# Kernel tuning notes

Measured on AMD Instinct MI355X. Metric: run time of the kernel, lower is better.

The kernel has to match this reference:

```python
import jax, jax.numpy as jnp
import numpy as np

N = 30000
E = 600000
IN = 64
HID = 128
EPS = 1e-5
HEADS_PER_LAYER = (4, 4, 1)


def _bn(x, g, b):
    # eval-mode BatchNorm: running_mean=0, running_var=1
    return x * (g / np.sqrt(1.0 + EPS)) + b


def _segment_softmax(e, dst, n):
    m = jax.ops.segment_max(e, dst, num_segments=n)
    ex = jnp.exp(e - m[dst])
    s = jax.ops.segment_sum(ex, dst, num_segments=n)
    return ex / (s[dst] + 1e-16)


def _gcn_conv(x, w, b, src, dst, norm, n):
    m = (x @ w)[src] * norm[:, None]            # [E+N, HID]
    return jax.ops.segment_sum(m, dst, num_segments=n) + b


def _gat_conv(x, w, a_src, a_dst, b, src, dst, n, heads):
    C = HID // heads
    xh = (x @ w).reshape(n, heads, C)
    asrc = (xh * a_src.reshape(heads, C)).sum(-1)   # [N, heads]
    adst = (xh * a_dst.reshape(heads, C)).sum(-1)
    e = jax.nn.leaky_relu(asrc[src] + adst[dst], 0.2)  # [E+N, heads]
    alpha = _segment_softmax(e, dst, n)
    out = jax.ops.segment_sum(xh[src] * alpha[:, :, None], dst, num_segments=n)
    return out.reshape(n, HID) + b


def _forward(x, gcn_in_w, gcn_in_b, gcn_res_w, gcn_res_b, gcn_w, gcn_b,
             gcn_bn_g, gcn_bn_b, gcn_c1w, gcn_c1b, gcn_c2w, gcn_c2b,
             gcn_c3w, gcn_c3b, gat_in_w, gat_in_b, gat_w, gat_asrc,
             gat_adst, gat_b, gat_bn_g, gat_bn_b, feat_imp, gat_c1w,
             gat_c1b, gat_cbn_g, gat_cbn_b, gat_c2w, gat_c2b, gat_c3w,
             gat_c3b, fin_w, fin_b, fin_bn_g, fin_bn_b, fin2_w, fin2_b,
             edge_index):
    n = x.shape[0]
    loop = jnp.arange(n, dtype=edge_index.dtype)
    src = jnp.concatenate([edge_index[0], loop])  # add self-loops
    dst = jnp.concatenate([edge_index[1], loop])
    # GCN symmetric normalization (with self-loops)
    deg = jax.ops.segment_sum(jnp.ones_like(dst, dtype=x.dtype), dst, num_segments=n)
    dis = jnp.where(deg > 0, jax.lax.rsqrt(jnp.maximum(deg, 1.0)), 0.0)
    norm = dis[src] * dis[dst]

    # ---- GCN branch (eval: dropout = identity, self-attn skipped since N>5000) ----
    xp = x @ gcn_in_w + gcn_in_b
    res = x @ gcn_res_w + gcn_res_b
    for i in range(3):
        xn = _gcn_conv(xp, gcn_w[i], gcn_b[i], src, dst, norm, n)
        xn = jax.nn.relu(_bn(xn, gcn_bn_g[i], gcn_bn_b[i]))
        if i % 2 == 1:
            xp = xn + res
            res = xp
        else:
            xp = xn
    h = jax.nn.relu(xp @ gcn_c1w + gcn_c1b)
    h = jax.nn.relu(h @ gcn_c2w + gcn_c2b)
    gcn_out = h @ gcn_c3w + gcn_c3b

    # ---- GAT branch ----
    xg = x @ gat_in_w + gat_in_b
    for i in range(3):
        xg = _gat_conv(xg, gat_w[i], gat_asrc[i], gat_adst[i], gat_b[i],
                       src, dst, n, HEADS_PER_LAYER[i])
        xg = jax.nn.elu(_bn(xg, gat_bn_g[i], gat_bn_b[i]))
    xg = xg * feat_imp
    h = jax.nn.relu(xg @ gat_c1w + gat_c1b)
    h = _bn(h, gat_cbn_g, gat_cbn_b)
    h = jax.nn.relu(h @ gat_c2w + gat_c2b)
    gat_out = h @ gat_c3w + gat_c3b

    # ---- fusion: N > 10000 -> weighted blend path ----
    fused = 0.6 * gcn_out + 0.4 * gat_out
    h = jax.nn.relu(fused @ fin_w + fin_b)
    h = _bn(h, fin_bn_g, fin_bn_b)
    return h @ fin2_w + fin2_b  # [N, 2]


def setup_inputs() -> dict:
    key = jax.random.key(0)
    ks = iter(jax.random.split(key, 64))

    def nrm(shape, scale=1.0):
        return jax.random.normal(next(ks), shape, dtype=jnp.float32) * scale

    s_in = 1.0 / np.sqrt(IN)
    s_h = 1.0 / np.sqrt(HID)
    inp = {}
    inp['x'] = nrm((N, IN))
    inp['edge_index'] = jax.random.randint(next(ks), (2, E), 0, N, dtype=jnp.int32)
    inp['gcn_in_w'] = nrm((IN, HID), s_in); inp['gcn_in_b'] = nrm((HID,), 0.01)
    inp['gcn_res_w'] = nrm((IN, HID), s_in); inp['gcn_res_b'] = nrm((HID,), 0.01)
    inp['gcn_w'] = nrm((3, HID, HID), s_h); inp['gcn_b'] = nrm((3, HID), 0.01)
    inp['gcn_bn_g'] = 1.0 + nrm((3, HID), 0.1); inp['gcn_bn_b'] = nrm((3, HID), 0.1)
    inp['gcn_c1w'] = nrm((HID, 64), s_h); inp['gcn_c1b'] = nrm((64,), 0.01)
    inp['gcn_c2w'] = nrm((64, 32), 0.125); inp['gcn_c2b'] = nrm((32,), 0.01)
    inp['gcn_c3w'] = nrm((32, HID), 0.18); inp['gcn_c3b'] = nrm((HID,), 0.01)
    inp['gat_in_w'] = nrm((IN, HID), s_in); inp['gat_in_b'] = nrm((HID,), 0.01)
    inp['gat_w'] = nrm((3, HID, HID), s_h)
    inp['gat_asrc'] = nrm((3, HID), s_h); inp['gat_adst'] = nrm((3, HID), s_h)
    inp['gat_b'] = nrm((3, HID), 0.01)
    inp['gat_bn_g'] = 1.0 + nrm((3, HID), 0.1); inp['gat_bn_b'] = nrm((3, HID), 0.1)
    inp['feat_imp'] = 1.0 + nrm((HID,), 0.1)
    inp['gat_c1w'] = nrm((HID, 64), s_h); inp['gat_c1b'] = nrm((64,), 0.01)
    inp['gat_cbn_g'] = 1.0 + nrm((64,), 0.1); inp['gat_cbn_b'] = nrm((64,), 0.1)
    inp['gat_c2w'] = nrm((64, 32), 0.125); inp['gat_c2b'] = nrm((32,), 0.01)
    inp['gat_c3w'] = nrm((32, HID), 0.18); inp['gat_c3b'] = nrm((HID,), 0.01)
    inp['fin_w'] = nrm((HID, 64), s_h); inp['fin_b'] = nrm((64,), 0.01)
    inp['fin_bn_g'] = 1.0 + nrm((64,), 0.1); inp['fin_bn_b'] = nrm((64,), 0.1)
    inp['fin2_w'] = nrm((64, 2), 0.125); inp['fin2_b'] = nrm((2,), 0.01)
    return inp


def reference(x, edge_index, gcn_in_w, gcn_in_b, gcn_res_w, gcn_res_b, gcn_w,
              gcn_b, gcn_bn_g, gcn_bn_b, gcn_c1w, gcn_c1b, gcn_c2w, gcn_c2b,
              gcn_c3w, gcn_c3b, gat_in_w, gat_in_b, gat_w, gat_asrc, gat_adst,
              gat_b, gat_bn_g, gat_bn_b, feat_imp, gat_c1w, gat_c1b, gat_cbn_g,
              gat_cbn_b, gat_c2w, gat_c2b, gat_c3w, gat_c3b, fin_w, fin_b,
              fin_bn_g, fin_bn_b, fin2_w, fin2_b):
    return _forward(x, gcn_in_w, gcn_in_b, gcn_res_w, gcn_res_b, gcn_w, gcn_b,
                    gcn_bn_g, gcn_bn_b, gcn_c1w, gcn_c1b, gcn_c2w, gcn_c2b,
                    gcn_c3w, gcn_c3b, gat_in_w, gat_in_b, gat_w, gat_asrc,
                    gat_adst, gat_b, gat_bn_g, gat_bn_b, feat_imp, gat_c1w,
                    gat_c1b, gat_cbn_g, gat_cbn_b, gat_c2w, gat_c2b, gat_c3w,
                    gat_c3b, fin_w, fin_b, fin_bn_g, fin_bn_b, fin2_w, fin2_b,
                    edge_index)
```

## Files before the change

### kernel.cpp

```cpp
#include <hip/hip_runtime.h>
#include <hip/hip_fp16.h>

#define RSQ_BN 0.9999950000374997f

typedef _Float16 f16x8 __attribute__((ext_vector_type(8)));
typedef float f32x4 __attribute__((ext_vector_type(4)));

union H8u { uint4 u4; __half h[8]; };
union H4u { uint2 u2; __half h[4]; };

__device__ __forceinline__ float leaky02(float x) { return x > 0.f ? x : 0.2f * x; }

__device__ __forceinline__ float4 ld4(const float* p) {
    return *reinterpret_cast<const float4*>(p);
}
__device__ __forceinline__ void ld8(float* d, const float* p) {
    float4 u = ld4(p), v = ld4(p + 4);
    d[0] = u.x; d[1] = u.y; d[2] = u.z; d[3] = u.w;
    d[4] = v.x; d[5] = v.y; d[6] = v.z; d[7] = v.w;
}


__global__ void hist_k(const int* __restrict__ edst, int* __restrict__ cnt, int E, int EN) {
    int i = blockIdx.x * 256 + threadIdx.x;
    if (i >= EN) return;
    int d = (i < E) ? edst[i] : (i - E);
    atomicAdd(&cnt[d], 1);
}

__global__ __launch_bounds__(256)
void scanA_k(const int* __restrict__ cnt, int* __restrict__ rowptr,
             int* __restrict__ bsum, int n) {
    __shared__ int sh[256];
    int t = threadIdx.x;
    int i = blockIdx.x * 256 + t;
    int v = (i < n) ? cnt[i] : 0;
    sh[t] = v;
    __syncthreads();
#pragma unroll
    for (int off = 1; off < 256; off <<= 1) {
        int u = 0;
        if (t >= off) u = sh[t - off];
        __syncthreads();
        sh[t] += u;
        __syncthreads();
    }
    if (i < n) rowptr[i] = sh[t] - v;
    if (t == 255) bsum[blockIdx.x] = sh[255];
}

__global__ __launch_bounds__(256)
void scanB_k(int* __restrict__ bsum, int nb) {
    __shared__ int sh[256];
    int t = threadIdx.x;
    int v = (t < nb) ? bsum[t] : 0;
    sh[t] = v;
    __syncthreads();
#pragma unroll
    for (int off = 1; off < 256; off <<= 1) {
        int u = 0;
        if (t >= off) u = sh[t - off];
        __syncthreads();
        sh[t] += u;
        __syncthreads();
    }
    if (t < nb) bsum[t] = sh[t] - v;
}

__global__ __launch_bounds__(256)
void scanC_k(const int* __restrict__ cnt, const int* __restrict__ bsum,
             int* __restrict__ rowptr, int* __restrict__ cursor,
             float* __restrict__ dis, int n, int EN) {
    int i = blockIdx.x * 256 + threadIdx.x;
    if (i < n) {
        int r = rowptr[i] + bsum[blockIdx.x];
        rowptr[i] = r;
        cursor[i] = r;
        dis[i] = rsqrtf((float)cnt[i]);
    }
    if (i == 0) rowptr[n] = EN;
}

__global__ void scatter_k(const int* __restrict__ esrc, const int* __restrict__ edst,
                          int* __restrict__ cursor, int* __restrict__ colidx, int E, int EN) {
    int i = blockIdx.x * 256 + threadIdx.x;
    if (i >= EN) return;
    int s, d;
    if (i < E) { s = esrc[i]; d = edst[i]; }
    else       { s = i - E; d = s; }
    int pos = atomicAdd(&cursor[d], 1);
    colidx[pos] = s;
}


__global__ void wtx_all_k(const float* __restrict__ gcn_in_w, const float* __restrict__ gcn_res_w,
                          const float* __restrict__ gat_in_w,
                          const float* __restrict__ gcn_w, const float* __restrict__ gat_w,
                          const float* __restrict__ gcn_c1w, const float* __restrict__ gat_c1w,
                          const float* __restrict__ gcn_c3w, const float* __restrict__ gat_c3w,
                          const float* __restrict__ fin_w,
                          const float* __restrict__ gcn_c2w, const float* __restrict__ gat_c2w,
                          const float* __restrict__ gat_asrc, const float* __restrict__ gat_adst,
                          __half* __restrict__ WTin, __half* __restrict__ WTg,
                          __half* __restrict__ WTa, __half* __restrict__ WTc1,
                          __half* __restrict__ WTc3, __half* __restrict__ WTfin,
                          __half* __restrict__ WTc2, __half* __restrict__ WTd) {
    int idx = blockIdx.x * 256 + threadIdx.x;
    const float* src;
    __half* dst;
    int K, M, o;
    if (idx < 24576) {
        int mi = idx >> 13; o = idx & 8191;
        src = mi == 0 ? gcn_in_w : (mi == 1 ? gcn_res_w : gat_in_w);
        dst = WTin + mi * 8192; K = 64; M = 128;
    } else if (idx < 73728) {
        int r = idx - 24576; int mi = r >> 14; o = r & 16383;
        src = gcn_w + mi * 16384; dst = WTg + mi * 16384; K = 128; M = 128;
    } else if (idx < 122880) {
        int r = idx - 73728; int mi = r >> 14; o = r & 16383;
        src = gat_w + mi * 16384; dst = WTa + mi * 16384; K = 128; M = 128;
    } else if (idx < 139264) {
        int r = idx - 122880; int mi = r >> 13; o = r & 8191;
        src = mi ? gat_c1w : gcn_c1w; dst = WTc1 + mi * 8192; K = 128; M = 64;
    } else if (idx < 147456) {
        int r = idx - 139264; int mi = r >> 12; o = r & 4095;
        src = mi ? gat_c3w : gcn_c3w; dst = WTc3 + mi * 4096; K = 32; M = 128;
    } else if (idx < 155648) {
        o = idx - 147456; src = fin_w; dst = WTfin; K = 128; M = 64;
    } else if (idx < 159744) {
        int r = idx - 155648; int mi = r >> 11; o = r & 2047;
        src = mi ? gat_c2w : gcn_c2w; dst = WTc2 + mi * 2048; K = 64; M = 32;
    } else if (idx < 165888) {
        int r = idx - 159744;
        int layer = r >> 11; o = r & 2047;
        int col = o >> 7, k = o & 127;
        int hh = (layer < 2) ? 4 : 1;
        int C = 128 / hh;
        float v = 0.f;
        if (col < hh) {
            const float* w = gat_w + (size_t)(layer * 128 + k) * 128 + col * C;
            const float* av = gat_asrc + layer * 128 + col * C;
            for (int c2 = 0; c2 < C; ++c2) v += w[c2] * av[c2];
        } else if (col >= 8 && col < 8 + hh) {
            int hthis = col - 8;
            const float* w = gat_w + (size_t)(layer * 128 + k) * 128 + hthis * C;
            const float* av = gat_adst + layer * 128 + hthis * C;
            for (int c2 = 0; c2 < C; ++c2) v += w[c2] * av[c2];
        }
        WTd[(size_t)layer * 2048 + o] = (__half)v;
        return;
    } else return;
    int mcol = o / K, k = o - mcol * K;
    dst[o] = (__half)src[k * M + mcol];
}


__device__ __forceinline__ f16x8 mk_af(const float* xr, int kb) {
    float4 v0 = ld4(xr + kb), v1 = ld4(xr + kb + 4);
    f16x8 af;
    af[0] = (_Float16)v0.x; af[1] = (_Float16)v0.y;
    af[2] = (_Float16)v0.z; af[3] = (_Float16)v0.w;
    af[4] = (_Float16)v1.x; af[5] = (_Float16)v1.y;
    af[6] = (_Float16)v1.z; af[7] = (_Float16)v1.w;
    return af;
}

__global__ __launch_bounds__(256)
void mfma_lin3_k(const float* __restrict__ X, const __half* __restrict__ WTin,
                 const float* __restrict__ b0, __half* __restrict__ Y0,
                 const float* __restrict__ b1, __half* __restrict__ Y1,
                 const float* __restrict__ b2, __half* __restrict__ Y2,
                 int n, int gper) {
    constexpr int K = 64, CT = 8;
    int set = blockIdx.x / gper, blk = blockIdx.x % gper;
    const __half* WT = WTin + (size_t)set * 8192;
    const float* bi = set == 0 ? b0 : (set == 1 ? b1 : b2);
    __half* Y = set == 0 ? Y0 : (set == 1 ? Y1 : Y2);
    int wave = threadIdx.x >> 6, lane = threadIdx.x & 63;
    int m = lane & 15, quad = lane >> 4;
    int row0 = blk * 64 + wave * 16;
    int arow = min(row0 + m, n - 1);
    const float* xr = X + (size_t)arow * K;
    f32x4 acc[CT];
#pragma unroll
    for (int ct = 0; ct < CT; ++ct) acc[ct] = (f32x4){0.f, 0.f, 0.f, 0.f};
#pragma unroll
    for (int k32 = 0; k32 < K / 32; ++k32) {
        int kb = k32 * 32 + quad * 8;
        f16x8 af = mk_af(xr, kb);
#pragma unroll
        for (int ct = 0; ct < CT; ++ct) {
            f16x8 bf = *reinterpret_cast<const f16x8*>(WT + (size_t)(ct * 16 + m) * K + kb);
            acc[ct] = __builtin_amdgcn_mfma_f32_16x16x32_f16(bf, af, acc[ct], 0, 0, 0);
        }
    }
    int row = row0 + m;
    if (row < n) {
#pragma unroll
        for (int ct = 0; ct < CT; ++ct) {
            int col = ct * 16 + quad * 4;
            float4 bv = ld4(bi + col);
            H4u w;
            w.h[0] = (__half)(acc[ct][0] + bv.x);
            w.h[1] = (__half)(acc[ct][1] + bv.y);
            w.h[2] = (__half)(acc[ct][2] + bv.z);
            w.h[3] = (__half)(acc[ct][3] + bv.w);
            *reinterpret_cast<uint2*>(Y + (size_t)row * 128 + col) = w.u2;
        }
    }
}


__global__ __launch_bounds__(256)
void dual128_mfma_k(const __half* __restrict__ Xg, const __half* __restrict__ WTg,
                    __half* __restrict__ Yg,
                    const __half* __restrict__ Xa, const __half* __restrict__ WTa,
                    __half* __restrict__ Ya,
                    const float* __restrict__ dis,
                    const __half* __restrict__ WTd,
                    float* __restrict__ avp, float* __restrict__ bvp,
                    int hh, int n, int gper) {
    bool gat = blockIdx.x >= gper;
    int blk = gat ? blockIdx.x - gper : blockIdx.x;
    const __half* X = gat ? Xa : Xg;
    const __half* WT = gat ? WTa : WTg;
    __half* Y = gat ? Ya : Yg;
    int wave = threadIdx.x >> 6;
    int lane = threadIdx.x & 63;
    int m = lane & 15, quad = lane >> 4;
    int row0 = blk * 64 + wave * 16;
    int arow = min(row0 + m, n - 1);
    const __half* xr = X + (size_t)arow * 128;
    f32x4 acc[8];
#pragma unroll
    for (int ct = 0; ct < 8; ++ct) acc[ct] = (f32x4){0.f, 0.f, 0.f, 0.f};
    int row = row0 + m;
    if (!gat) {
#pragma unroll
        for (int k32 = 0; k32 < 4; ++k32) {
            int kb = k32 * 32 + quad * 8;
            f16x8 af = *reinterpret_cast<const f16x8*>(xr + kb);
#pragma unroll
            for (int ct = 0; ct < 8; ++ct) {
                f16x8 bf = *reinterpret_cast<const f16x8*>(WT + (size_t)(ct * 16 + m) * 128 + kb);
                acc[ct] = __builtin_amdgcn_mfma_f32_16x16x32_f16(bf, af, acc[ct], 0, 0, 0);
            }
        }
        if (row < n) {
            float dv = dis[row];
#pragma unroll
            for (int ct = 0; ct < 8; ++ct) {
                int col = ct * 16 + quad * 4;
                H4u w;
                w.h[0] = (__half)(acc[ct][0] * dv);
                w.h[1] = (__half)(acc[ct][1] * dv);
                w.h[2] = (__half)(acc[ct][2] * dv);
                w.h[3] = (__half)(acc[ct][3] * dv);
                *reinterpret_cast<uint2*>(Y + (size_t)row * 128 + col) = w.u2;
            }
        }
    } else {
        f32x4 accd = (f32x4){0.f, 0.f, 0.f, 0.f};
#pragma unroll
        for (int k32 = 0; k32 < 4; ++k32) {
            int kb = k32 * 32 + quad * 8;
            f16x8 af = *reinterpret_cast<const f16x8*>(xr + kb);
#pragma unroll
            for (int ct = 0; ct < 8; ++ct) {
                f16x8 bf = *reinterpret_cast<const f16x8*>(WT + (size_t)(ct * 16 + m) * 128 + kb);
                acc[ct] = __builtin_amdgcn_mfma_f32_16x16x32_f16(bf, af, acc[ct], 0, 0, 0);
            }
            f16x8 bd = *reinterpret_cast<const f16x8*>(WTd + (size_t)m * 128 + kb);
            accd = __builtin_amdgcn_mfma_f32_16x16x32_f16(bd, af, accd, 0, 0, 0);
        }
        if (row < n) {
#pragma unroll
            for (int ct = 0; ct < 8; ++ct) {
                int col = ct * 16 + quad * 4;
                H4u w;
                w.h[0] = (__half)acc[ct][0];
                w.h[1] = (__half)acc[ct][1];
                w.h[2] = (__half)acc[ct][2];
                w.h[3] = (__half)acc[ct][3];
                *reinterpret_cast<uint2*>(Y + (size_t)row * 128 + col) = w.u2;
            }
            if (quad == 0) {
#pragma unroll
                for (int reg = 0; reg < 4; ++reg)
                    if (reg < hh) avp[row * hh + reg] = accd[reg];
            } else if (quad == 2) {
#pragma unroll
                for (int reg = 0; reg < 4; ++reg)
                    if (reg < hh) bvp[row * hh + reg] = accd[reg];
            }
        }
    }
}


__global__ __launch_bounds__(256)
void fused_gather_k(const int* __restrict__ rowptr, const int* __restrict__ colidx,
                    const float* __restrict__ dis,
                    const __half* __restrict__ Tg, const float* __restrict__ gbias,
                    const float* __restrict__ gbng, const float* __restrict__ gbnb,
                    const __half* __restrict__ res, __half* __restrict__ Yg,
                    const __half* __restrict__ Ta, const float* __restrict__ avp,
                    const float* __restrict__ bvp, const float* __restrict__ abias,
                    const float* __restrict__ abng, const float* __restrict__ abnb,
                    const float* __restrict__ fimp, __half* __restrict__ Ya,
                    int n, int hh, int log2C) {
    int idx = blockIdx.x * 256 + threadIdx.x;
    int i = idx >> 4;
    if (i >= n) return;
    int c = (idx & 15) * 8;
    int h = c >> log2C;
    float ad = bvp[i * hh + h];
    int p0 = rowptr[i], p1 = rowptr[i + 1];
    float g[8], a[8];
#pragma unroll
    for (int t = 0; t < 8; ++t) { g[t] = 0.f; a[t] = 0.f; }
    float m = -3.0e38f, s = 0.f;

    int ng = (p1 - p0 + 3) >> 2;
    int p = p0;
    int sx[4]; float av[4], vm[4];
#pragma unroll
    for (int j = 0; j < 4; ++j) {
        int q = p0 + j;
        vm[j] = (q < p1) ? 1.f : 0.f;
        sx[j] = colidx[min(q, p1 - 1)];
    }
#pragma unroll
    for (int j = 0; j < 4; ++j) av[j] = avp[sx[j] * hh + h];

    for (int gi = 0; gi < ng; ++gi) {
        uint4 qg[4], qa[4];
#pragma unroll
        for (int j = 0; j < 4; ++j)
            qg[j] = *reinterpret_cast<const uint4*>(Tg + (size_t)sx[j] * 128 + c);
#pragma unroll
        for (int j = 0; j < 4; ++j)
            qa[j] = *reinterpret_cast<const uint4*>(Ta + (size_t)sx[j] * 128 + c);
        int pn = p + 4;
        int sn[4]; float avn[4], vmn[4];
#pragma unroll
        for (int j = 0; j < 4; ++j) {
            int q = pn + j;
            vmn[j] = (q < p1) ? 1.f : 0.f;
            sn[j] = colidx[min(max(q, p0), p1 - 1)];
        }
#pragma unroll
        for (int j = 0; j < 4; ++j) avn[j] = avp[sn[j] * hh + h];
        float e0 = vm[0] > 0.f ? leaky02(av[0] + ad) : -3.0e38f;
        float e1 = vm[1] > 0.f ? leaky02(av[1] + ad) : -3.0e38f;
        float e2 = vm[2] > 0.f ? leaky02(av[2] + ad) : -3.0e38f;
        float e3 = vm[3] > 0.f ? leaky02(av[3] + ad) : -3.0e38f;
        float mc = fmaxf(fmaxf(e0, e1), fmaxf(e2, e3));
        float mn = fmaxf(m, mc);
        float scale = __expf(m - mn);
        float w0 = __expf(e0 - mn), w1 = __expf(e1 - mn);
        float w2 = __expf(e2 - mn), w3 = __expf(e3 - mn);
        s = s * scale + (w0 + w1 + w2 + w3);
        m = mn;
        {
            H8u k0, k1, k2, k3;
            k0.u4 = qg[0]; k1.u4 = qg[1]; k2.u4 = qg[2]; k3.u4 = qg[3];
#pragma unroll
            for (int t = 0; t < 8; ++t) {
                float v = g[t];
                v = fmaf(__half2float(k0.h[t]), vm[0], v);
                v = fmaf(__half2float(k1.h[t]), vm[1], v);
                v = fmaf(__half2float(k2.h[t]), vm[2], v);
                v = fmaf(__half2float(k3.h[t]), vm[3], v);
                g[t] = v;
            }
        }
        {
            H8u k0, k1, k2, k3;
            k0.u4 = qa[0]; k1.u4 = qa[1]; k2.u4 = qa[2]; k3.u4 = qa[3];
#pragma unroll
            for (int t = 0; t < 8; ++t) {
                float v = a[t] * scale;
                v = fmaf(__half2float(k0.h[t]), w0, v);
                v = fmaf(__half2float(k1.h[t]), w1, v);
                v = fmaf(__half2float(k2.h[t]), w2, v);
                v = fmaf(__half2float(k3.h[t]), w3, v);
                a[t] = v;
            }
        }
        p = pn;
#pragma unroll
        for (int j = 0; j < 4; ++j) { sx[j] = sn[j]; av[j] = avn[j]; vm[j] = vmn[j]; }
    }

    {
        float di = dis[i];
        float bb[8], gg[8], nb[8];
        ld8(bb, gbias + c); ld8(gg, gbng + c); ld8(nb, gbnb + c);
        float o[8];
#pragma unroll
        for (int t = 0; t < 8; ++t) {
            float v = g[t] * di + bb[t];
            o[t] = fmaxf(v * (gg[t] * RSQ_BN) + nb[t], 0.f);
        }
        if (res) {
            H8u rr;
            rr.u4 = *reinterpret_cast<const uint4*>(res + (size_t)i * 128 + c);
#pragma unroll
            for (int t = 0; t < 8; ++t) o[t] += __half2float(rr.h[t]);
        }
        H8u w;
#pragma unroll
        for (int t = 0; t < 8; ++t) w.h[t] = (__half)o[t];
        *reinterpret_cast<uint4*>(Yg + (size_t)i * 128 + c) = w.u4;
    }
    {
        float si = 1.f / (s + 1e-16f);
        float bb[8], gg[8], nb[8];
        ld8(bb, abias + c); ld8(gg, abng + c); ld8(nb, abnb + c);
        float o[8];
#pragma unroll
        for (int t = 0; t < 8; ++t) {
            float v = a[t] * si + bb[t];
            v = v * (gg[t] * RSQ_BN) + nb[t];
            o[t] = v > 0.f ? v : expm1f(v);
        }
        if (fimp) {
            float ff[8]; ld8(ff, fimp + c);
#pragma unroll
            for (int t = 0; t < 8; ++t) o[t] *= ff[t];
        }
        H8u w;
#pragma unroll
        for (int t = 0; t < 8; ++t) w.h[t] = (__half)o[t];
        *reinterpret_cast<uint4*>(Ya + (size_t)i * 128 + c) = w.u4;
    }
}


__global__ __launch_bounds__(256)
void fused_tail_k(const __half* __restrict__ Xg, const __half* __restrict__ Xa,
                  const __half* __restrict__ WTc1,
                  const float* __restrict__ c1bg, const float* __restrict__ c1ba,
                  const float* __restrict__ cbng, const float* __restrict__ cbnb,
                  const __half* __restrict__ WTc2,
                  const float* __restrict__ c2bg, const float* __restrict__ c2ba,
                  const __half* __restrict__ WTc3,
                  const float* __restrict__ c3bg, const float* __restrict__ c3ba,
                  const __half* __restrict__ WTfin, const float* __restrict__ finb,
                  const float* __restrict__ fbng, const float* __restrict__ fbnb,
                  const float* __restrict__ w2, const float* __restrict__ b2,
                  float* __restrict__ out, int n) {
    __shared__ alignas(16) __half h1s[2][64][88];
    __shared__ alignas(16) __half h2s[2][64][56];
    __shared__ alignas(16) __half Fs[64][152];
    int wave = threadIdx.x >> 6, lane = threadIdx.x & 63;
    int m = lane & 15, quad = lane >> 4;
    int row0 = blockIdx.x * 64 + wave * 16;
    int lr0 = wave * 16;
    int arow = min(row0 + m, n - 1);

#pragma unroll
    for (int br = 0; br < 2; ++br) {
        const __half* xr = (br ? Xa : Xg) + (size_t)arow * 128;
        const __half* WT = WTc1 + br * 8192;
        f32x4 acc[4];
#pragma unroll
        for (int ct = 0; ct < 4; ++ct) acc[ct] = (f32x4){0.f, 0.f, 0.f, 0.f};
#pragma unroll
        for (int k32 = 0; k32 < 4; ++k32) {
            int kb = k32 * 32 + quad * 8;
            f16x8 af = *reinterpret_cast<const f16x8*>(xr + kb);
#pragma unroll
            for (int ct = 0; ct < 4; ++ct) {
                f16x8 bf = *reinterpret_cast<const f16x8*>(WT + (ct * 16 + m) * 128 + kb);
                acc[ct] = __builtin_amdgcn_mfma_f32_16x16x32_f16(af, bf, acc[ct], 0, 0, 0);
            }
        }
        const float* bi = br ? c1ba : c1bg;
#pragma unroll
        for (int ct = 0; ct < 4; ++ct) {
            int col = ct * 16 + m;
            float cb = bi[col];
            float cg = br ? cbng[col] * RSQ_BN : 1.f;
            float cbb = br ? cbnb[col] : 0.f;
#pragma unroll
            for (int reg = 0; reg < 4; ++reg) {
                float v = fmaxf(acc[ct][reg] + cb, 0.f) * cg + cbb;
                h1s[br][lr0 + quad * 4 + reg][col] = (__half)v;
            }
        }
    }
    __syncthreads();
#pragma unroll
    for (int br = 0; br < 2; ++br) {
        f32x4 acc[2];
        acc[0] = (f32x4){0.f, 0.f, 0.f, 0.f};
        acc[1] = (f32x4){0.f, 0.f, 0.f, 0.f};
        const __half* WT = WTc2 + br * 2048;
#pragma unroll
        for (int k32 = 0; k32 < 2; ++k32) {
            int kb = k32 * 32 + quad * 8;
            f16x8 af = *reinterpret_cast<const f16x8*>(&h1s[br][lr0 + m][kb]);
#pragma unroll
            for (int ct = 0; ct < 2; ++ct) {
                f16x8 bf = *reinterpret_cast<const f16x8*>(WT + (ct * 16 + m) * 64 + kb);
                acc[ct] = __builtin_amdgcn_mfma_f32_16x16x32_f16(af, bf, acc[ct], 0, 0, 0);
            }
        }
        const float* bi = br ? c2ba : c2bg;
#pragma unroll
        for (int ct = 0; ct < 2; ++ct) {
            int col = ct * 16 + m;
            float cb = bi[col];
#pragma unroll
            for (int reg = 0; reg < 4; ++reg) {
                float v = fmaxf(acc[ct][reg] + cb, 0.f);
                h2s[br][lr0 + quad * 4 + reg][col] = (__half)v;
            }
        }
    }
    __syncthreads();
    {
        f32x4 ag[8], aa[8];
#pragma unroll
        for (int ct = 0; ct < 8; ++ct) {
            ag[ct] = (f32x4){0.f, 0.f, 0.f, 0.f};
            aa[ct] = (f32x4){0.f, 0.f, 0.f, 0.f};
        }
        int kb = quad * 8;
        f16x8 afg = *reinterpret_cast<const f16x8*>(&h2s[0][lr0 + m][kb]);
        f16x8 afa = *reinterpret_cast<const f16x8*>(&h2s[1][lr0 + m][kb]);
#pragma unroll
        for (int ct = 0; ct < 8; ++ct) {
            f16x8 bfg = *reinterpret_cast<const f16x8*>(WTc3 + (ct * 16 + m) * 32 + kb);
            f16x8 bfa = *reinterpret_cast<const f16x8*>(WTc3 + 4096 + (ct * 16 + m) * 32 + kb);
            ag[ct] = __builtin_amdgcn_mfma_f32_16x16x32_f16(afg, bfg, ag[ct], 0, 0, 0);
            aa[ct] = __builtin_amdgcn_mfma_f32_16x16x32_f16(afa, bfa, aa[ct], 0, 0, 0);
        }
#pragma unroll
        for (int ct = 0; ct < 8; ++ct) {
            int col = ct * 16 + m;
            float cb = 0.6f * c3bg[col] + 0.4f * c3ba[col];
#pragma unroll
            for (int reg = 0; reg < 4; ++reg) {
                float v = 0.6f * ag[ct][reg] + 0.4f * aa[ct][reg] + cb;
                Fs[lr0 + quad * 4 + reg][col] = (__half)v;
            }
        }
    }
    __syncthreads();
    {
        f32x4 acc[4];
#pragma unroll
        for (int ct = 0; ct < 4; ++ct) acc[ct] = (f32x4){0.f, 0.f, 0.f, 0.f};
#pragma unroll
        for (int k32 = 0; k32 < 4; ++k32) {
            int kb = k32 * 32 + quad * 8;
            f16x8 af = *reinterpret_cast<const f16x8*>(&Fs[lr0 + m][kb]);
#pragma unroll
            for (int ct = 0; ct < 4; ++ct) {
                f16x8 bf = *reinterpret_cast<const f16x8*>(WTfin + (ct * 16 + m) * 128 + kb);
                acc[ct] = __builtin_amdgcn_mfma_f32_16x16x32_f16(af, bf, acc[ct], 0, 0, 0);
            }
        }
        float p0[4] = {0.f, 0.f, 0.f, 0.f}, p1[4] = {0.f, 0.f, 0.f, 0.f};
#pragma unroll
        for (int ct = 0; ct < 4; ++ct) {
            int col = ct * 16 + m;
            float cb = finb[col];
            float cg = fbng[col] * RSQ_BN;
            float cbb = fbnb[col];
            float w20 = w2[2 * col], w21 = w2[2 * col + 1];
#pragma unroll
            for (int reg = 0; reg < 4; ++reg) {
                float v = fmaxf(acc[ct][reg] + cb, 0.f) * cg + cbb;
                p0[reg] += v * w20;
                p1[reg] += v * w21;
            }
        }
        for (int off = 1; off < 16; off <<= 1) {
#pragma unroll
            for (int reg = 0; reg < 4; ++reg) {
                p0[reg] += __shfl_xor(p0[reg], off);
                p1[reg] += __shfl_xor(p1[reg], off);
            }
        }
        if (m == 0) {
#pragma unroll
            for (int reg = 0; reg < 4; ++reg) {
                int row = row0 + quad * 4 + reg;
                if (row < n) {
                    out[row * 2] = p0[reg] + b2[0];
                    out[row * 2 + 1] = p1[reg] + b2[1];
                }
            }
        }
    }
}


static inline int cdiv(int a, int b) { return (a + b - 1) / b; }

extern "C" void kernel_launch(void* const* d_in, const int* in_sizes, int n_in,
                              void* d_out, int out_size, void* d_ws, size_t ws_size,
                              hipStream_t stream) {
    const float* x       = (const float*)d_in[0];
    const int*   ei      = (const int*)d_in[1];
    const float* gcn_in_w = (const float*)d_in[2];
    const float* gcn_in_b = (const float*)d_in[3];
    const float* gcn_res_w = (const float*)d_in[4];
    const float* gcn_res_b = (const float*)d_in[5];
    const float* gcn_w   = (const float*)d_in[6];
    const float* gcn_b   = (const float*)d_in[7];
    const float* gcn_bn_g = (const float*)d_in[8];
    const float* gcn_bn_b = (const float*)d_in[9];
    const float* gcn_c1w = (const float*)d_in[10];
    const float* gcn_c1b = (const float*)d_in[11];
    const float* gcn_c2w = (const float*)d_in[12];
    const float* gcn_c2b = (const float*)d_in[13];
    const float* gcn_c3w = (const float*)d_in[14];
    const float* gcn_c3b = (const float*)d_in[15];
    const float* gat_in_w = (const float*)d_in[16];
    const float* gat_in_b = (const float*)d_in[17];
    const float* gat_w   = (const float*)d_in[18];
    const float* gat_asrc = (const float*)d_in[19];
    const float* gat_adst = (const float*)d_in[20];
    const float* gat_b   = (const float*)d_in[21];
    const float* gat_bn_g = (const float*)d_in[22];
    const float* gat_bn_b = (const float*)d_in[23];
    const float* feat_imp = (const float*)d_in[24];
    const float* gat_c1w = (const float*)d_in[25];
    const float* gat_c1b = (const float*)d_in[26];
    const float* gat_cbn_g = (const float*)d_in[27];
    const float* gat_cbn_b = (const float*)d_in[28];
    const float* gat_c2w = (const float*)d_in[29];
    const float* gat_c2b = (const float*)d_in[30];
    const float* gat_c3w = (const float*)d_in[31];
    const float* gat_c3b = (const float*)d_in[32];
    const float* fin_w   = (const float*)d_in[33];
    const float* fin_b   = (const float*)d_in[34];
    const float* fin_bn_g = (const float*)d_in[35];
    const float* fin_bn_b = (const float*)d_in[36];
    const float* fin2_w  = (const float*)d_in[37];
    const float* fin2_b  = (const float*)d_in[38];

    const int N = in_sizes[0] / 64;
    const int E = in_sizes[1] / 2;
    const int EN = E + N;
    const int* esrc = ei;
    const int* edst = ei + E;

    char* wp = (char*)d_ws;
    auto alloc = [&](size_t bytes) -> void* {
        void* p = (void*)wp;
        wp += (bytes + 255) & ~(size_t)255;
        return p;
    };
    int* cnt    = (int*)alloc((size_t)N * 4);
    int* rowptr = (int*)alloc((size_t)(N + 1) * 4);
    int* cursor = (int*)alloc((size_t)N * 4);
    int* bsum   = (int*)alloc((size_t)256 * 4);
    int* colidx = (int*)alloc((size_t)EN * 4);
    float* dis  = (float*)alloc((size_t)N * 4);
    __half* A   = (__half*)alloc((size_t)N * 128 * 2);
    __half* B   = (__half*)alloc((size_t)N * 128 * 2);
    __half* G   = (__half*)alloc((size_t)N * 128 * 2);
    __half* H   = (__half*)alloc((size_t)N * 128 * 2);
    __half* R   = (__half*)alloc((size_t)N * 128 * 2);
    __half* Th1 = (__half*)alloc((size_t)N * 128 * 2);
    __half* Th2 = (__half*)alloc((size_t)N * 128 * 2);
    float* avv  = (float*)alloc((size_t)N * 4 * 4);
    float* bvv  = (float*)alloc((size_t)N * 4 * 4);
    __half* WTin = (__half*)alloc((size_t)3 * 8192 * 2);
    __half* WTg  = (__half*)alloc((size_t)3 * 16384 * 2);
    __half* WTa  = (__half*)alloc((size_t)3 * 16384 * 2);
    __half* WTc1 = (__half*)alloc((size_t)2 * 8192 * 2);
    __half* WTc3 = (__half*)alloc((size_t)2 * 4096 * 2);
    __half* WTfin = (__half*)alloc((size_t)8192 * 2);
    __half* WTc2 = (__half*)alloc((size_t)2 * 2048 * 2);
    __half* WTd  = (__half*)alloc((size_t)3 * 2048 * 2);

    const int nScanB = cdiv(N, 256);
    hipMemsetAsync(cnt, 0, (size_t)N * 4, stream);
    hist_k<<<cdiv(EN, 256), 256, 0, stream>>>(edst, cnt, E, EN);
    scanA_k<<<nScanB, 256, 0, stream>>>(cnt, rowptr, bsum, N);
    scanB_k<<<1, 256, 0, stream>>>(bsum, nScanB);
    scanC_k<<<nScanB, 256, 0, stream>>>(cnt, bsum, rowptr, cursor, dis, N, EN);
    scatter_k<<<cdiv(EN, 256), 256, 0, stream>>>(esrc, edst, cursor, colidx, E, EN);
    wtx_all_k<<<648, 256, 0, stream>>>(gcn_in_w, gcn_res_w, gat_in_w, gcn_w, gat_w,
                                       gcn_c1w, gat_c1w, gcn_c3w, gat_c3w, fin_w,
                                       gcn_c2w, gat_c2w, gat_asrc, gat_adst,
                                       WTin, WTg, WTa, WTc1, WTc3, WTfin, WTc2, WTd);

    const int g64r = cdiv(N, 64);
    const int gG   = cdiv(N, 16);

    mfma_lin3_k<<<3 * g64r, 256, 0, stream>>>(x, WTin, gcn_in_b, A, gcn_res_b, R,
                                              gat_in_b, G, N, g64r);

    const int heads_arr[3] = {4, 4, 1};
    __half* gcur = A; __half* gnxt = B;
    __half* acur = G; __half* anxt = H;
    for (int i = 0; i < 3; ++i) {
        int hh = heads_arr[i];
        int log2C = (hh == 4) ? 5 : 7;
        dual128_mfma_k<<<2 * g64r, 256, 0, stream>>>(gcur, WTg + (size_t)i * 16384, Th1,
                                                     acur, WTa + (size_t)i * 16384, Th2, dis,
                                                     WTd + (size_t)i * 2048,
                                                     avv, bvv, hh, N, g64r);
        fused_gather_k<<<gG, 256, 0, stream>>>(rowptr, colidx, dis,
                                               Th1, gcn_b + i * 128, gcn_bn_g + i * 128,
                                               gcn_bn_b + i * 128, (i == 1) ? R : nullptr, gnxt,
                                               Th2, avv, bvv, gat_b + i * 128,
                                               gat_bn_g + i * 128, gat_bn_b + i * 128,
                                               (i == 2) ? feat_imp : nullptr, anxt,
                                               N, hh, log2C);
        __half* t = gcur; gcur = gnxt; gnxt = t;
        t = acur; acur = anxt; anxt = t;
    }

    fused_tail_k<<<g64r, 256, 0, stream>>>(gcur, acur,
                                           WTc1, gcn_c1b, gat_c1b, gat_cbn_g, gat_cbn_b,
                                           WTc2, gcn_c2b, gat_c2b,
                                           WTc3, gcn_c3b, gat_c3b,
                                           WTfin, fin_b, fin_bn_g, fin_bn_b,
                                           fin2_w, fin2_b, (float*)d_out, N);
}
```

Measured before the change: 472.5 us.

## Pre-swizzle weights into MFMA fragment order and double-buffer edge gathers

Weight transposition now writes fp16 weights in per-lane MFMA fragment order, so every B-fragment load in the GEMM kernels becomes one contiguous 16-byte read per lane indexed by lane, replacing strided row reads. Separately, the fused GAT/GCN gather loop is restructured into two alternating register buffers (A/B), so the next group's feature gathers are issued before the current group is processed. This aims to improve weight-load coalescing and hide gather latency, at the cost of more registers and a loop that rounds up to even group counts and handles the padded groups through masking.

```diff
diff --git a/kernel.cpp b/kernel.cpp
--- a/kernel.cpp
+++ b/kernel.cpp
@@ -133,7 +133,9 @@
     } else if (idx < 165888) {
         int r = idx - 159744;
         int layer = r >> 11; o = r & 2047;
-        int col = o >> 7, k = o & 127;
+        int j = o & 7, lane = (o >> 3) & 63, k32 = o >> 9;
+        int col = lane & 15, quad = lane >> 4;
+        int k = k32 * 32 + quad * 8 + j;
         int hh = (layer < 2) ? 4 : 1;
         int C = 128 / hh;
         float v = 0.f;
@@ -150,7 +152,12 @@
         WTd[(size_t)layer * 2048 + o] = (__half)v;
         return;
     } else return;
-    int mcol = o / K, k = o - mcol * K;
+    int j = o & 7, lane = (o >> 3) & 63, r = o >> 9;
+    int KD32 = K >> 5;
+    int ct = r / KD32, k32 = r - ct * KD32;
+    int m = lane & 15, quad = lane >> 4;
+    int k = k32 * 32 + quad * 8 + j;
+    int mcol = ct * 16 + m;
     dst[o] = (__half)src[k * M + mcol];
 }
 
@@ -190,7 +197,7 @@
         f16x8 af = mk_af(xr, kb);
 #pragma unroll
         for (int ct = 0; ct < CT; ++ct) {
-            f16x8 bf = *reinterpret_cast<const f16x8*>(WT + (size_t)(ct * 16 + m) * K + kb);
+            f16x8 bf = *reinterpret_cast<const f16x8*>(WT + ((ct * 2 + k32) << 9) + (lane << 3));
             acc[ct] = __builtin_amdgcn_mfma_f32_16x16x32_f16(bf, af, acc[ct], 0, 0, 0);
         }
     }
@@ -242,7 +249,7 @@
             f16x8 af = *reinterpret_cast<const f16x8*>(xr + kb);
 #pragma unroll
             for (int ct = 0; ct < 8; ++ct) {
-                f16x8 bf = *reinterpret_cast<const f16x8*>(WT + (size_t)(ct * 16 + m) * 128 + kb);
+                f16x8 bf = *reinterpret_cast<const f16x8*>(WT + ((ct * 4 + k32) << 9) + (lane << 3));
                 acc[ct] = __builtin_amdgcn_mfma_f32_16x16x32_f16(bf, af, acc[ct], 0, 0, 0);
             }
         }
@@ -267,10 +274,10 @@
             f16x8 af = *reinterpret_cast<const f16x8*>(xr + kb);
 #pragma unroll
             for (int ct = 0; ct < 8; ++ct) {
-                f16x8 bf = *reinterpret_cast<const f16x8*>(WT + (size_t)(ct * 16 + m) * 128 + kb);
+                f16x8 bf = *reinterpret_cast<const f16x8*>(WT + ((ct * 4 + k32) << 9) + (lane << 3));
                 acc[ct] = __builtin_amdgcn_mfma_f32_16x16x32_f16(bf, af, acc[ct], 0, 0, 0);
             }
-            f16x8 bd = *reinterpret_cast<const f16x8*>(WTd + (size_t)m * 128 + kb);
+            f16x8 bd = *reinterpret_cast<const f16x8*>(WTd + (k32 << 9) + (lane << 3));
             accd = __builtin_amdgcn_mfma_f32_16x16x32_f16(bd, af, accd, 0, 0, 0);
         }
         if (row < n) {
@@ -297,6 +304,68 @@
     }
 }
 
+
+__device__ __forceinline__ void gidx(const int* __restrict__ colidx,
+                                     const float* __restrict__ avp, int base,
+                                     int p0, int p1, int hh, int h,
+                                     int* SX, float* AV, float* VM) {
+#pragma unroll
+    for (int j = 0; j < 4; ++j) {
+        int q = base + j;
+        VM[j] = (q < p1) ? 1.f : 0.f;
+        SX[j] = colidx[min(max(q, p0), p1 - 1)];
+    }
+#pragma unroll
+    for (int j = 0; j < 4; ++j) AV[j] = avp[SX[j] * hh + h];
+}
+
+__device__ __forceinline__ void ggath(const __half* __restrict__ Tg,
+                                      const __half* __restrict__ Ta, int c,
+                                      const int* SX, uint4* QG, uint4* QA) {
+#pragma unroll
+    for (int j = 0; j < 4; ++j)
+        QG[j] = *reinterpret_cast<const uint4*>(Tg + (size_t)SX[j] * 128 + c);
+#pragma unroll
+    for (int j = 0; j < 4; ++j)
+        QA[j] = *reinterpret_cast<const uint4*>(Ta + (size_t)SX[j] * 128 + c);
+}
+
+__device__ __forceinline__ void gproc(const uint4* QG, const uint4* QA,
+                                      const float* AV, const float* VM, float ad,
+                                      float& m, float& s, float* g, float* a) {
+    float e0 = VM[0] > 0.f ? leaky02(AV[0] + ad) : -3.0e38f;
+    float e1 = VM[1] > 0.f ? leaky02(AV[1] + ad) : -3.0e38f;
+    float e2 = VM[2] > 0.f ? leaky02(AV[2] + ad) : -3.0e38f;
+    float e3 = VM[3] > 0.f ? leaky02(AV[3] + ad) : -3.0e38f;
+    float mc = fmaxf(fmaxf(e0, e1), fmaxf(e2, e3));
+    float mn = fmaxf(m, mc);
+    float scale = __expf(m - mn);
+    float w0 = __expf(e0 - mn), w1 = __expf(e1 - mn);
+    float w2 = __expf(e2 - mn), w3 = __expf(e3 - mn);
+    s = s * scale + (w0 + w1 + w2 + w3);
+    m = mn;
+    H8u k0, k1, k2, k3;
+    k0.u4 = QG[0]; k1.u4 = QG[1]; k2.u4 = QG[2]; k3.u4 = QG[3];
+#pragma unroll
+    for (int t = 0; t < 8; ++t) {
+        float v = g[t];
+        v = fmaf(__half2float(k0.h[t]), VM[0], v);
+        v = fmaf(__half2float(k1.h[t]), VM[1], v);
+        v = fmaf(__half2float(k2.h[t]), VM[2], v);
+        v = fmaf(__half2float(k3.h[t]), VM[3], v);
+        g[t] = v;
+    }
+    k0.u4 = QA[0]; k1.u4 = QA[1]; k2.u4 = QA[2]; k3.u4 = QA[3];
+#pragma unroll
+    for (int t = 0; t < 8; ++t) {
+        float v = a[t] * scale;
+        v = fmaf(__half2float(k0.h[t]), w0, v);
+        v = fmaf(__half2float(k1.h[t]), w1, v);
+        v = fmaf(__half2float(k2.h[t]), w2, v);
+        v = fmaf(__half2float(k3.h[t]), w3, v);
+        a[t] = v;
+    }
+}
 
 __global__ __launch_bounds__(256)
 void fused_gather_k(const int* __restrict__ rowptr, const int* __restrict__ colidx,
@@ -322,75 +391,23 @@
     float m = -3.0e38f, s = 0.f;
 
     int ng = (p1 - p0 + 3) >> 2;
-    int p = p0;
-    int sx[4]; float av[4], vm[4];
-#pragma unroll
-    for (int j = 0; j < 4; ++j) {
-        int q = p0 + j;
-        vm[j] = (q < p1) ? 1.f : 0.f;
-        sx[j] = colidx[min(q, p1 - 1)];
-    }
-#pragma unroll
-    for (int j = 0; j < 4; ++j) av[j] = avp[sx[j] * hh + h];
-
-    for (int gi = 0; gi < ng; ++gi) {
-        uint4 qg[4], qa[4];
-#pragma unroll
-        for (int j = 0; j < 4; ++j)
-            qg[j] = *reinterpret_cast<const uint4*>(Tg + (size_t)sx[j] * 128 + c);
-#pragma unroll
-        for (int j = 0; j < 4; ++j)
-            qa[j] = *reinterpret_cast<const uint4*>(Ta + (size_t)sx[j] * 128 + c);
-        int pn = p + 4;
-        int sn[4]; float avn[4], vmn[4];
-#pragma unroll
-        for (int j = 0; j < 4; ++j) {
-            int q = pn + j;
-            vmn[j] = (q < p1) ? 1.f : 0.f;
-            sn[j] = colidx[min(max(q, p0), p1 - 1)];
-        }
-#pragma unroll
-        for (int j = 0; j < 4; ++j) avn[j] = avp[sn[j] * hh + h];
-        float e0 = vm[0] > 0.f ? leaky02(av[0] + ad) : -3.0e38f;
-        float e1 = vm[1] > 0.f ? leaky02(av[1] + ad) : -3.0e38f;
-        float e2 = vm[2] > 0.f ? leaky02(av[2] + ad) : -3.0e38f;
-        float e3 = vm[3] > 0.f ? leaky02(av[3] + ad) : -3.0e38f;
-        float mc = fmaxf(fmaxf(e0, e1), fmaxf(e2, e3));
-        float mn = fmaxf(m, mc);
-        float scale = __expf(m - mn);
-        float w0 = __expf(e0 - mn), w1 = __expf(e1 - mn);
-        float w2 = __expf(e2 - mn), w3 = __expf(e3 - mn);
-        s = s * scale + (w0 + w1 + w2 + w3);
-        m = mn;
-        {
-            H8u k0, k1, k2, k3;
-            k0.u4 = qg[0]; k1.u4 = qg[1]; k2.u4 = qg[2]; k3.u4 = qg[3];
-#pragma unroll
-            for (int t = 0; t < 8; ++t) {
-                float v = g[t];
-                v = fmaf(__half2float(k0.h[t]), vm[0], v);
-                v = fmaf(__half2float(k1.h[t]), vm[1], v);
-                v = fmaf(__half2float(k2.h[t]), vm[2], v);
-                v = fmaf(__half2float(k3.h[t]), vm[3], v);
-                g[t] = v;
-            }
-        }
-        {
-            H8u k0, k1, k2, k3;
-            k0.u4 = qa[0]; k1.u4 = qa[1]; k2.u4 = qa[2]; k3.u4 = qa[3];
-#pragma unroll
-            for (int t = 0; t < 8; ++t) {
-                float v = a[t] * scale;
-                v = fmaf(__half2float(k0.h[t]), w0, v);
-                v = fmaf(__half2float(k1.h[t]), w1, v);
-                v = fmaf(__half2float(k2.h[t]), w2, v);
-                v = fmaf(__half2float(k3.h[t]), w3, v);
-                a[t] = v;
-            }
-        }
-        p = pn;
-#pragma unroll
-        for (int j = 0; j < 4; ++j) { sx[j] = sn[j]; av[j] = avn[j]; vm[j] = vmn[j]; }
+    int ng2 = (ng + 1) & ~1;
+
+    int sxA[4], sxB[4];
+    float avA[4], vmA[4], avB[4], vmB[4];
+    uint4 qgA[4], qaA[4], qgB[4], qaB[4];
+
+    gidx(colidx, avp, p0, p0, p1, hh, h, sxA, avA, vmA);
+    ggath(Tg, Ta, c, sxA, qgA, qaA);
+    gidx(colidx, avp, p0 + 4, p0, p1, hh, h, sxB, avB, vmB);
+
+    for (int gi = 0; gi < ng2; gi += 2) {
+        ggath(Tg, Ta, c, sxB, qgB, qaB);
+        gproc(qgA, qaA, avA, vmA, ad, m, s, g, a);
+        gidx(colidx, avp, p0 + (gi + 2) * 4, p0, p1, hh, h, sxA, avA, vmA);
+        ggath(Tg, Ta, c, sxA, qgA, qaA);
+        gproc(qgB, qaB, avB, vmB, ad, m, s, g, a);
+        gidx(colidx, avp, p0 + (gi + 3) * 4, p0, p1, hh, h, sxB, avB, vmB);
     }
 
     {
@@ -473,7 +490,7 @@
             f16x8 af = *reinterpret_cast<const f16x8*>(xr + kb);
 #pragma unroll
             for (int ct = 0; ct < 4; ++ct) {
-                f16x8 bf = *reinterpret_cast<const f16x8*>(WT + (ct * 16 + m) * 128 + kb);
+                f16x8 bf = *reinterpret_cast<const f16x8*>(WT + ((ct * 4 + k32) << 9) + (lane << 3));
                 acc[ct] = __builtin_amdgcn_mfma_f32_16x16x32_f16(af, bf, acc[ct], 0, 0, 0);
             }
         }
@@ -504,7 +521,7 @@
             f16x8 af = *reinterpret_cast<const f16x8*>(&h1s[br][lr0 + m][kb]);
 #pragma unroll
             for (int ct = 0; ct < 2; ++ct) {
-                f16x8 bf = *reinterpret_cast<const f16x8*>(WT + (ct * 16 + m) * 64 + kb);
+                f16x8 bf = *reinterpret_cast<const f16x8*>(WT + ((ct * 2 + k32) << 9) + (lane << 3));
                 acc[ct] = __builtin_amdgcn_mfma_f32_16x16x32_f16(af, bf, acc[ct], 0, 0, 0);
             }
         }
@@ -533,8 +550,8 @@
         f16x8 afa = *reinterpret_cast<const f16x8*>(&h2s[1][lr0 + m][kb]);
 #pragma unroll
         for (int ct = 0; ct < 8; ++ct) {
-            f16x8 bfg = *reinterpret_cast<const f16x8*>(WTc3 + (ct * 16 + m) * 32 + kb);
-            f16x8 bfa = *reinterpret_cast<const f16x8*>(WTc3 + 4096 + (ct * 16 + m) * 32 + kb);
+            f16x8 bfg = *reinterpret_cast<const f16x8*>(WTc3 + (ct << 9) + (lane << 3));
+            f16x8 bfa = *reinterpret_cast<const f16x8*>(WTc3 + 4096 + (ct << 9) + (lane << 3));
             ag[ct] = __builtin_amdgcn_mfma_f32_16x16x32_f16(afg, bfg, ag[ct], 0, 0, 0);
             aa[ct] = __builtin_amdgcn_mfma_f32_16x16x32_f16(afa, bfa, aa[ct], 0, 0, 0);
         }
@@ -560,7 +577,7 @@
             f16x8 af = *reinterpret_cast<const f16x8*>(&Fs[lr0 + m][kb]);
 #pragma unroll
             for (int ct = 0; ct < 4; ++ct) {
-                f16x8 bf = *reinterpret_cast<const f16x8*>(WTfin + (ct * 16 + m) * 128 + kb);
+                f16x8 bf = *reinterpret_cast<const f16x8*>(WTfin + ((ct * 4 + k32) << 9) + (lane << 3));
                 acc[ct] = __builtin_amdgcn_mfma_f32_16x16x32_f16(af, bf, acc[ct], 0, 0, 0);
             }
         }
```

Result: faster. 438.4 us (-7.2%).
